# Performance work log

Measured on AMD Instinct MI355X. Metric: run time of the kernel, lower is better.

## Reference

```python
import jax, jax.numpy as jnp
import numpy as np

DIM = 1024
LN_EPS = 1e-5


def setup_inputs() -> dict:
    key = jax.random.key(0)
    ks = jax.random.split(key, 6)
    B, S, D = 8, 2048, DIM
    x = jax.random.normal(ks[0], (B, S, D), dtype=jnp.float32)
    mask = jnp.ones((B, S, 1), dtype=jnp.float32)
    # LayerNorm params
    ln_g = jnp.ones((D,), dtype=jnp.float32)
    ln_b = jnp.zeros((D,), dtype=jnp.float32)
    # FeedForward: Linear(D, D) -> GELU -> Linear(D, D); hidden_dim == dim per source
    lim = 1.0 / np.sqrt(D)
    w1 = jax.random.uniform(ks[1], (D, D), jnp.float32, -lim, lim)
    b1 = jax.random.uniform(ks[2], (D,), jnp.float32, -lim, lim)
    w2 = jax.random.uniform(ks[3], (D, D), jnp.float32, -lim, lim)
    b2 = jax.random.uniform(ks[4], (D,), jnp.float32, -lim, lim)
    return {"x": x, "mask": mask, "ln_g": ln_g, "ln_b": ln_b,
            "w1": w1, "b1": b1, "w2": w2, "b2": b2}


def _layernorm(t, g, b):
    mu = jnp.mean(t, axis=-1, keepdims=True)
    var = jnp.mean(jnp.square(t - mu), axis=-1, keepdims=True)
    return (t - mu) * jax.lax.rsqrt(var + LN_EPS) * g + b


def reference(x, mask, ln_g, ln_b, w1, b1, w2, b2):
    # torch.fft(t, signal_ndim=1): FFT over hidden axis (complex input, imag=0)
    ft = jnp.fft.fft(x.astype(jnp.float32), axis=-1)
    # torch.fft(., signal_ndim=2): 2D FFT over (seq, hidden)
    ft = jnp.fft.fft2(ft, axes=(-2, -1))
    ft = ft.real  # [..., 0] slice of the fake-complex tensor
    t = _layernorm(x + ft, ln_g, ln_b)
    # FeedForward: Linear -> GELU(exact) -> Linear (dropout is identity at eval)
    h = jax.nn.gelu(t @ w1 + b1, approximate=False)
    out = h @ w2 + b2
    return out * mask
```

## Files before the change

kernel.cpp:

```cpp
#include <hip/hip_runtime.h>
#include <math.h>

#define DIMD 1024
#define SEQ  2048
#define BATCH 8
#define ROWS (BATCH * SEQ)

#define MF 1152
#define KF 1088

typedef __attribute__((ext_vector_type(8))) short bf16x8;
typedef __attribute__((ext_vector_type(4))) float f32x4;
typedef __attribute__((ext_vector_type(8))) unsigned short ushort8;

__device__ __forceinline__ unsigned short f2bf(float f) {
    unsigned u = __float_as_uint(f);
    unsigned r = (u + 0x7FFFu + ((u >> 16) & 1u)) >> 16;
    return (unsigned short)r;
}
__device__ __forceinline__ float bf2f(unsigned short h) {
    return __uint_as_float(((unsigned)h) << 16);
}
__device__ __forceinline__ void gl_lds16(const void* g, void* l) {
    __builtin_amdgcn_global_load_lds(
        (const __attribute__((address_space(1))) unsigned int*)g,
        (__attribute__((address_space(3))) unsigned int*)l, 16, 0, 0);
}


__global__ __launch_bounds__(256) void build_acos(unsigned short* __restrict__ Acos) {
    int s = blockIdx.x;
    for (int t = threadIdx.x; t < KF; t += 256) {
        float c = 0.0f;
        if (t <= 1024) {
            int prod = (s * t) & (SEQ - 1);
            c = 1024.0f * cospif((float)prod * (1.0f / 1024.0f));
        }
        Acos[(size_t)s * KF + t] = f2bf(c);
    }
}

__global__ __launch_bounds__(256) void build_xe(const float* __restrict__ x,
                                                unsigned short* __restrict__ Xe) {
    int lane = threadIdx.x & 63;
    int oct  = threadIdx.x >> 6;
    int n = blockIdx.x * 64 + lane;
    int b = n >> 10, d = n & 1023;
    int rd = (DIMD - d) & (DIMD - 1);
    int t0 = blockIdx.y * 32 + oct * 8;
    const float* xb = x + (size_t)b * SEQ * DIMD + rd;
    ushort8 tmp;
    #pragma unroll
    for (int j = 0; j < 8; ++j) {
        int t = t0 + j;
        float v;
        if (t == 0)          v = xb[0];
        else if (t < 1024)   v = xb[(size_t)t * DIMD] + xb[(size_t)(2048 - t) * DIMD];
        else if (t == 1024)  v = xb[(size_t)1024 * DIMD];
        else                 v = 0.0f;
        tmp[j] = f2bf(v);
    }
    *(ushort8*)&Xe[(size_t)n * KF + t0] = tmp;
}

__global__ __launch_bounds__(256) void pack_wt(const float* __restrict__ W,
                                               unsigned short* __restrict__ Wt) {
    int lane = threadIdx.x & 63;
    int oct = threadIdx.x >> 6;
    int n = blockIdx.x * 64 + lane;
    int k0 = blockIdx.y * 32 + oct * 8;
    ushort8 tmp;
    #pragma unroll
    for (int j = 0; j < 8; ++j) tmp[j] = f2bf(W[(size_t)(k0 + j) * DIMD + n]);
    *(ushort8*)&Wt[(size_t)n * DIMD + k0] = tmp;
}

template <int MODE>
__global__ __launch_bounds__(256) void gemm_bt(const unsigned short* __restrict__ A,
                                               const unsigned short* __restrict__ B,
                                               int K, int lda, int ldb, int ldc,
                                               const float* __restrict__ bias,
                                               const float* __restrict__ mask,
                                               void* __restrict__ outp) {
    __shared__ unsigned short As[128 * 64];
    __shared__ unsigned short Bs[128 * 64];

    const int tid = threadIdx.x;
    const int lane = tid & 63;
    const int wv = tid >> 6;
    const int wm = wv & 1;
    const int wn = wv >> 1;
    const int fr = lane & 15;
    const int quad = lane >> 4;

    int bx = blockIdx.x, by = blockIdx.y;
    if (MODE != 0) {
        int lin = bx + 8 * by;
        int c = lin & 7;
        int g = lin >> 3;
        bx = g & 7;
        by = (g >> 3) * 8 + c;
    }
    const int m0 = by * 128;
    const int n0 = bx * 128;

    const int st_row = (lane >> 3);
    const int st_col = ((lane & 7) ^ st_row) * 8;

    f32x4 acc[4][4] = {};

    for (int k0 = 0; k0 < K; k0 += 64) {
        __syncthreads();
        #pragma unroll
        for (int i = 0; i < 4; ++i) {
            int chunk = wv * 4 + i;
            int ar = m0 + chunk * 8 + st_row;
            int br = n0 + chunk * 8 + st_row;
            gl_lds16(&A[(size_t)ar * lda + k0 + st_col], &As[chunk * 512]);
            gl_lds16(&B[(size_t)br * ldb + k0 + st_col], &Bs[chunk * 512]);
        }
        __syncthreads();

        const int sw = fr & 7;
        #pragma unroll
        for (int ks = 0; ks < 2; ++ks) {
            const int slot = (ks * 4 + quad) ^ sw;
            bf16x8 af[4], bfv[4];
            #pragma unroll
            for (int i = 0; i < 4; ++i)
                af[i] = *(const bf16x8*)&As[(wm * 64 + i * 16 + fr) * 64 + slot * 8];
            #pragma unroll
            for (int j = 0; j < 4; ++j)
                bfv[j] = *(const bf16x8*)&Bs[(wn * 64 + j * 16 + fr) * 64 + slot * 8];
            #pragma unroll
            for (int i = 0; i < 4; ++i)
                #pragma unroll
                for (int j = 0; j < 4; ++j)
                    acc[i][j] = __builtin_amdgcn_mfma_f32_16x16x32_bf16(af[i], bfv[j], acc[i][j], 0, 0, 0);
        }
    }

    #pragma unroll
    for (int i = 0; i < 4; ++i) {
        int rowb = m0 + wm * 64 + i * 16 + quad * 4;
        #pragma unroll
        for (int j = 0; j < 4; ++j) {
            int col = n0 + wn * 64 + j * 16 + fr;
            #pragma unroll
            for (int r = 0; r < 4; ++r) {
                float v = acc[i][j][r];
                int row = rowb + r;
                if (MODE == 0) {
                    ((float*)outp)[(size_t)row * ldc + col] = v;
                } else if (MODE == 1) {
                    v += bias[col];
                    v = 0.5f * v * (1.0f + erff(v * 0.70710678118654752f));
                    ((unsigned short*)outp)[(size_t)row * ldc + col] = f2bf(v);
                } else {
                    v += bias[col];
                    v *= mask[row];
                    ((float*)outp)[(size_t)row * ldc + col] = v;
                }
            }
        }
    }
}

__global__ __launch_bounds__(256) void ln_pair(const float* __restrict__ x,
                                               const float* __restrict__ F,
                                               const float* __restrict__ g,
                                               const float* __restrict__ beta,
                                               unsigned short* __restrict__ t) {
    const int sp = blockIdx.x;
    const int b  = blockIdx.y;

    float4 fv = ((const float4*)(F + (size_t)sp * 8192 + (size_t)b * 1024))[threadIdx.x];
    float4 g4 = ((const float4*)g)[threadIdx.x];
    float4 b4 = ((const float4*)beta)[threadIdx.x];

    __shared__ float red[4];
    const int wave = threadIdx.x >> 6;
    const int lane = threadIdx.x & 63;

    const int nrows = (sp >= 1 && sp <= 1023) ? 2 : 1;
    for (int p = 0; p < nrows; ++p) {
        int s = p ? (2048 - sp) : sp;
        int row = b * SEQ + s;
        float4 xv = ((const float4*)(x + (size_t)row * DIMD))[threadIdx.x];
        float v0 = xv.x + fv.x, v1 = xv.y + fv.y, v2 = xv.z + fv.z, v3 = xv.w + fv.w;

        float sm = v0 + v1 + v2 + v3;
        #pragma unroll
        for (int off = 32; off > 0; off >>= 1) sm += __shfl_down(sm, off, 64);
        if (lane == 0) red[wave] = sm;
        __syncthreads();
        const float mean = (red[0] + red[1] + red[2] + red[3]) * (1.0f / DIMD);

        float dx0 = v0 - mean, dx1 = v1 - mean, dx2 = v2 - mean, dx3 = v3 - mean;
        float q = dx0 * dx0 + dx1 * dx1 + dx2 * dx2 + dx3 * dx3;
        __syncthreads();
        #pragma unroll
        for (int off = 32; off > 0; off >>= 1) q += __shfl_down(q, off, 64);
        if (lane == 0) red[wave] = q;
        __syncthreads();
        const float var = (red[0] + red[1] + red[2] + red[3]) * (1.0f / DIMD);
        const float rstd = rsqrtf(var + 1e-5f);

        ushort4 o;
        o.x = f2bf(dx0 * rstd * g4.x + b4.x);
        o.y = f2bf(dx1 * rstd * g4.y + b4.y);
        o.z = f2bf(dx2 * rstd * g4.z + b4.z);
        o.w = f2bf(dx3 * rstd * g4.w + b4.w);
        ((ushort4*)(t + (size_t)row * DIMD))[threadIdx.x] = o;
        __syncthreads();
    }
}

#define BM 64
#define BN 64
#define BK 16

__global__ __launch_bounds__(256) void fft_cos_kernel(const float* __restrict__ x,
                                                      float* __restrict__ y) {
    __shared__ float tab[SEQ];
    __shared__ float As[BM][BK + 1];
    __shared__ float Bs[BK][BN + 1];
    const int tid = threadIdx.x;
    const int b = blockIdx.z;
    const int s0 = blockIdx.y * BM;
    const int n0 = blockIdx.x * BN;
    for (int i = tid; i < SEQ; i += 256) tab[i] = cospif((float)i * (1.0f / 1024.0f));
    const int tx = tid & 15;
    const int ty = tid >> 4;
    float acc[4][4] = {};
    const float* Xb = x + (size_t)b * SEQ * DIMD;
    for (int k0 = 0; k0 < SEQ; k0 += BK) {
        __syncthreads();
        for (int f = tid; f < BM * BK; f += 256) {
            int i = f / BK, k = f % BK;
            int prod = (s0 + i) * (k0 + k);
            As[i][k] = tab[prod & (SEQ - 1)];
        }
        for (int f = tid; f < BK * BN; f += 256) {
            int k = f / BN, j = f % BN;
            int d = n0 + j;
            int rd = (DIMD - d) & (DIMD - 1);
            Bs[k][j] = Xb[(size_t)(k0 + k) * DIMD + rd];
        }
        __syncthreads();
        #pragma unroll
        for (int k = 0; k < BK; ++k) {
            float a[4], bv[4];
            #pragma unroll
            for (int i = 0; i < 4; ++i) a[i] = As[ty * 4 + i][k];
            #pragma unroll
            for (int j = 0; j < 4; ++j) bv[j] = Bs[k][tx * 4 + j];
            #pragma unroll
            for (int i = 0; i < 4; ++i)
                #pragma unroll
                for (int j = 0; j < 4; ++j) acc[i][j] += a[i] * bv[j];
        }
    }
    #pragma unroll
    for (int i = 0; i < 4; ++i) {
        int s = s0 + ty * 4 + i;
        #pragma unroll
        for (int j = 0; j < 4; ++j) {
            int d = n0 + tx * 4 + j;
            y[((size_t)b * SEQ + s) * DIMD + d] = Xb[(size_t)s * DIMD + d] + 1024.0f * acc[i][j];
        }
    }
}

__global__ __launch_bounds__(256) void ln_kernel(float* __restrict__ y,
                                                 const float* __restrict__ g,
                                                 const float* __restrict__ beta) {
    const int row = blockIdx.x;
    float4* p = (float4*)(y + (size_t)row * DIMD);
    float4 v = p[threadIdx.x];
    __shared__ float red[4];
    const int wave = threadIdx.x >> 6;
    const int lane = threadIdx.x & 63;
    float s = v.x + v.y + v.z + v.w;
    #pragma unroll
    for (int off = 32; off > 0; off >>= 1) s += __shfl_down(s, off, 64);
    if (lane == 0) red[wave] = s;
    __syncthreads();
    const float mean = (red[0] + red[1] + red[2] + red[3]) * (1.0f / DIMD);
    float dx0 = v.x - mean, dx1 = v.y - mean, dx2 = v.z - mean, dx3 = v.w - mean;
    float q = dx0 * dx0 + dx1 * dx1 + dx2 * dx2 + dx3 * dx3;
    __syncthreads();
    #pragma unroll
    for (int off = 32; off > 0; off >>= 1) q += __shfl_down(q, off, 64);
    if (lane == 0) red[wave] = q;
    __syncthreads();
    const float var = (red[0] + red[1] + red[2] + red[3]) * (1.0f / DIMD);
    const float rstd = rsqrtf(var + 1e-5f);
    float4 g4 = ((const float4*)g)[threadIdx.x];
    float4 b4 = ((const float4*)beta)[threadIdx.x];
    float4 o;
    o.x = dx0 * rstd * g4.x + b4.x;
    o.y = dx1 * rstd * g4.y + b4.y;
    o.z = dx2 * rstd * g4.z + b4.z;
    o.w = dx3 * rstd * g4.w + b4.w;
    p[threadIdx.x] = o;
}

template <int MODE>
__global__ __launch_bounds__(256) void ff_gemm(const float* __restrict__ A,
                                               const float* __restrict__ W,
                                               const float* __restrict__ bias,
                                               const float* __restrict__ mask,
                                               float* __restrict__ out) {
    __shared__ float As[BM][BK + 1];
    __shared__ float Bs[BK][BN + 1];
    const int tid = threadIdx.x;
    const int tx = tid & 15;
    const int ty = tid >> 4;
    const int m0 = blockIdx.y * BM;
    const int n0 = blockIdx.x * BN;
    float acc[4][4] = {};
    for (int k0 = 0; k0 < DIMD; k0 += BK) {
        __syncthreads();
        for (int f = tid; f < BM * BK; f += 256) {
            int i = f / BK, k = f % BK;
            As[i][k] = A[(size_t)(m0 + i) * DIMD + k0 + k];
        }
        for (int f = tid; f < BK * BN; f += 256) {
            int k = f / BN, j = f % BN;
            Bs[k][j] = W[(size_t)(k0 + k) * DIMD + n0 + j];
        }
        __syncthreads();
        #pragma unroll
        for (int k = 0; k < BK; ++k) {
            float a[4], bv[4];
            #pragma unroll
            for (int i = 0; i < 4; ++i) a[i] = As[ty * 4 + i][k];
            #pragma unroll
            for (int j = 0; j < 4; ++j) bv[j] = Bs[k][tx * 4 + j];
            #pragma unroll
            for (int i = 0; i < 4; ++i)
                #pragma unroll
                for (int j = 0; j < 4; ++j) acc[i][j] += a[i] * bv[j];
        }
    }
    #pragma unroll
    for (int i = 0; i < 4; ++i) {
        int m = m0 + ty * 4 + i;
        float mk = (MODE == 1) ? mask[m] : 1.0f;
        #pragma unroll
        for (int j = 0; j < 4; ++j) {
            int n = n0 + tx * 4 + j;
            float v = acc[i][j] + bias[n];
            if (MODE == 0) v = 0.5f * v * (1.0f + erff(v * 0.70710678118654752f));
            else v *= mk;
            out[(size_t)m * DIMD + n] = v;
        }
    }
}

extern "C" void kernel_launch(void* const* d_in, const int* in_sizes, int n_in,
                              void* d_out, int out_size, void* d_ws, size_t ws_size,
                              hipStream_t stream) {
    const float* x    = (const float*)d_in[0];
    const float* mask = (const float*)d_in[1];
    const float* ln_g = (const float*)d_in[2];
    const float* ln_b = (const float*)d_in[3];
    const float* w1   = (const float*)d_in[4];
    const float* b1   = (const float*)d_in[5];
    const float* w2   = (const float*)d_in[6];
    const float* b2   = (const float*)d_in[7];
    float* out = (float*)d_out;

    const size_t MB = 1024 * 1024;
    dim3 blk(256);

    if (ws_size >= 70 * MB) {
        char* w = (char*)d_ws;
        unsigned short* Acos = (unsigned short*)w;
        unsigned short* Xe   = (unsigned short*)(w + 4 * MB);
        unsigned short* t    = (unsigned short*)(w + 32 * MB);
        unsigned short* h    = (unsigned short*)w;
        unsigned short* W1t  = (unsigned short*)(w + 64 * MB);
        unsigned short* W2t  = (unsigned short*)(w + 66 * MB);
        float* F = (float*)d_out;

        build_acos<<<dim3(MF), blk, 0, stream>>>(Acos);
        build_xe<<<dim3(8192 / 64, KF / 32), blk, 0, stream>>>(x, Xe);
        pack_wt<<<dim3(1024 / 64, 1024 / 32), blk, 0, stream>>>(w1, W1t);
        pack_wt<<<dim3(1024 / 64, 1024 / 32), blk, 0, stream>>>(w2, W2t);

        gemm_bt<0><<<dim3(8192 / 128, MF / 128), blk, 0, stream>>>(
            Acos, Xe, KF, KF, KF, 8192, nullptr, nullptr, F);
        ln_pair<<<dim3(1025, BATCH), blk, 0, stream>>>(x, F, ln_g, ln_b, t);
        gemm_bt<1><<<dim3(1024 / 128, ROWS / 128), blk, 0, stream>>>(
            t, W1t, 1024, 1024, 1024, 1024, b1, nullptr, h);
        gemm_bt<2><<<dim3(1024 / 128, ROWS / 128), blk, 0, stream>>>(
            h, W2t, 1024, 1024, 1024, 1024, b2, mask, out);
    } else {
        float* yf = (float*)d_ws;
        const size_t bufBytes = (size_t)ROWS * DIMD * sizeof(float);
        fft_cos_kernel<<<dim3(DIMD / BN, SEQ / BM, BATCH), blk, 0, stream>>>(x, yf);
        ln_kernel<<<dim3(ROWS), blk, 0, stream>>>(yf, ln_g, ln_b);
        ff_gemm<0><<<dim3(DIMD / BN, ROWS / BM), blk, 0, stream>>>(yf, w1, b1, nullptr, out);
        ff_gemm<1><<<dim3(DIMD / BN, ROWS / BM), blk, 0, stream>>>(out, w2, b2, mask, yf);
        hipMemcpyAsync(d_out, yf, bufBytes, hipMemcpyDeviceToDevice, stream);
    }
}
```

Measured before the change: 333.5 us.

## Replace 128x128 GEMM with 256x256 eight-wave ping-pong pipelined GEMM

Replaces the single-buffered 128x128-tile bf16 MFMA GEMM with a 512-thread, 256x256-tile kernel. It double-buffers LDS, interleaves global-to-LDS staging with MFMA phases, and uses explicit waitcnt, barriers and setprio. The DFT GEMM dimensions are padded to multiples of 256/128 (MF 1280, KF 1152) to fit the new tile, which adds some padded work. The intent is to hide load latency and raise data reuse per tile, at the cost of fewer blocks, higher LDS and register use, and fragile hand-tuned synchronisation.

New measurement: 321.8 us. 3.5% less time.

```diff
diff --git a/kernel.cpp b/kernel.cpp
--- a/kernel.cpp
+++ b/kernel.cpp
@@ -6,8 +6,8 @@
 #define BATCH 8
 #define ROWS (BATCH * SEQ)
 
-#define MF 1152
-#define KF 1088
+#define MF 1280
+#define KF 1152
 
 typedef __attribute__((ext_vector_type(8))) short bf16x8;
 typedef __attribute__((ext_vector_type(4))) float f32x4;
@@ -17,9 +17,6 @@
     unsigned u = __float_as_uint(f);
     unsigned r = (u + 0x7FFFu + ((u >> 16) & 1u)) >> 16;
     return (unsigned short)r;
-}
-__device__ __forceinline__ float bf2f(unsigned short h) {
-    return __uint_as_float(((unsigned)h) << 16);
 }
 __device__ __forceinline__ void gl_lds16(const void* g, void* l) {
     __builtin_amdgcn_global_load_lds(
@@ -76,88 +73,124 @@
 }
 
 template <int MODE>
-__global__ __launch_bounds__(256) void gemm_bt(const unsigned short* __restrict__ A,
-                                               const unsigned short* __restrict__ B,
-                                               int K, int lda, int ldb, int ldc,
-                                               const float* __restrict__ bias,
-                                               const float* __restrict__ mask,
-                                               void* __restrict__ outp) {
-    __shared__ unsigned short As[128 * 64];
-    __shared__ unsigned short Bs[128 * 64];
-
-    const int tid = threadIdx.x;
+__global__ __launch_bounds__(512, 2) void gemm8p(const unsigned short* __restrict__ A,
+                                                 const unsigned short* __restrict__ B,
+                                                 int K, int lda, int ldb, int ldc,
+                                                 const float* __restrict__ bias,
+                                                 const float* __restrict__ mask,
+                                                 void* __restrict__ outp) {
+    __shared__ unsigned short As[2][256 * 64];
+    __shared__ unsigned short Bs[2][256 * 64];
+
+    const int tid  = threadIdx.x;
     const int lane = tid & 63;
-    const int wv = tid >> 6;
-    const int wm = wv & 1;
-    const int wn = wv >> 1;
-    const int fr = lane & 15;
+    const int w    = tid >> 6;
+    const int wm   = w >> 2;
+    const int wn   = w & 3;
+    const int fr   = lane & 15;
     const int quad = lane >> 4;
+    const int sw   = fr & 7;
+
+    const int st_row = lane >> 3;
+    const int st_col = ((lane & 7) ^ st_row) * 8;
 
     int bx = blockIdx.x, by = blockIdx.y;
     if (MODE != 0) {
-        int lin = bx + 8 * by;
-        int c = lin & 7;
-        int g = lin >> 3;
-        bx = g & 7;
-        by = (g >> 3) * 8 + c;
-    }
-    const int m0 = by * 128;
-    const int n0 = bx * 128;
-
-    const int st_row = (lane >> 3);
-    const int st_col = ((lane & 7) ^ st_row) * 8;
-
-    f32x4 acc[4][4] = {};
-
-    for (int k0 = 0; k0 < K; k0 += 64) {
-        __syncthreads();
-        #pragma unroll
-        for (int i = 0; i < 4; ++i) {
-            int chunk = wv * 4 + i;
-            int ar = m0 + chunk * 8 + st_row;
-            int br = n0 + chunk * 8 + st_row;
-            gl_lds16(&A[(size_t)ar * lda + k0 + st_col], &As[chunk * 512]);
-            gl_lds16(&B[(size_t)br * ldb + k0 + st_col], &Bs[chunk * 512]);
-        }
-        __syncthreads();
-
-        const int sw = fr & 7;
-        #pragma unroll
-        for (int ks = 0; ks < 2; ++ks) {
-            const int slot = (ks * 4 + quad) ^ sw;
-            bf16x8 af[4], bfv[4];
-            #pragma unroll
-            for (int i = 0; i < 4; ++i)
-                af[i] = *(const bf16x8*)&As[(wm * 64 + i * 16 + fr) * 64 + slot * 8];
-            #pragma unroll
-            for (int j = 0; j < 4; ++j)
-                bfv[j] = *(const bf16x8*)&Bs[(wn * 64 + j * 16 + fr) * 64 + slot * 8];
-            #pragma unroll
-            for (int i = 0; i < 4; ++i)
-                #pragma unroll
-                for (int j = 0; j < 4; ++j)
-                    acc[i][j] = __builtin_amdgcn_mfma_f32_16x16x32_bf16(af[i], bfv[j], acc[i][j], 0, 0, 0);
-        }
-    }
-
-    #pragma unroll
-    for (int i = 0; i < 4; ++i) {
-        int rowb = m0 + wm * 64 + i * 16 + quad * 4;
-        #pragma unroll
-        for (int j = 0; j < 4; ++j) {
-            int col = n0 + wn * 64 + j * 16 + fr;
+        int lin = bx + 4 * by;
+        int c = lin & 7, r = lin >> 3;
+        by = c * 8 + (r >> 2);
+        bx = r & 3;
+    }
+    const int m0 = by * 256;
+    const int n0 = bx * 256;
+
+    auto stageA = [&](int buf, int qm, int kt) {
+        int kb = kt * 64 + st_col;
+        int c0 = qm * 8 + w;
+        int c1 = 16 + qm * 8 + w;
+        gl_lds16(&A[(size_t)(m0 + c0 * 8 + st_row) * lda + kb], &As[buf][c0 * 512]);
+        gl_lds16(&A[(size_t)(m0 + c1 * 8 + st_row) * lda + kb], &As[buf][c1 * 512]);
+    };
+    auto stageB = [&](int buf, int qn, int kt) {
+        int kb = kt * 64 + st_col;
+        int c0 = (w >> 1) * 8 + qn * 4 + (w & 1) * 2;
+        int c1 = c0 + 1;
+        gl_lds16(&B[(size_t)(n0 + c0 * 8 + st_row) * ldb + kb], &Bs[buf][c0 * 512]);
+        gl_lds16(&B[(size_t)(n0 + c1 * 8 + st_row) * ldb + kb], &Bs[buf][c1 * 512]);
+    };
+
+    f32x4 acc[8][4] = {};
+
+#define PHASE(BUF, QM, QN, STAGE, DOVM)                                              \
+    {                                                                                \
+        bf16x8 af[4][2], bv[2][2];                                                   \
+        _Pragma("unroll") for (int i = 0; i < 4; ++i) {                              \
+            const unsigned short* ab = &As[BUF][(wm * 128 + QM * 64 + i * 16 + fr) * 64]; \
+            _Pragma("unroll") for (int ks = 0; ks < 2; ++ks)                         \
+                af[i][ks] = *(const bf16x8*)&ab[((ks * 4 + quad) ^ sw) * 8];         \
+        }                                                                            \
+        _Pragma("unroll") for (int j = 0; j < 2; ++j) {                              \
+            const unsigned short* bb = &Bs[BUF][(wn * 64 + QN * 32 + j * 16 + fr) * 64]; \
+            _Pragma("unroll") for (int ks = 0; ks < 2; ++ks)                         \
+                bv[j][ks] = *(const bf16x8*)&bb[((ks * 4 + quad) ^ sw) * 8];         \
+        }                                                                            \
+        STAGE;                                                                       \
+        asm volatile("s_waitcnt lgkmcnt(8)");                                        \
+        __builtin_amdgcn_s_barrier();                                                \
+        asm volatile("s_waitcnt lgkmcnt(0)");                                        \
+        __builtin_amdgcn_s_setprio(1);                                               \
+        _Pragma("unroll") for (int i = 0; i < 4; ++i)                                \
+            _Pragma("unroll") for (int j = 0; j < 2; ++j)                            \
+                _Pragma("unroll") for (int ks = 0; ks < 2; ++ks)                     \
+                    acc[QM * 4 + i][QN * 2 + j] = __builtin_amdgcn_mfma_f32_16x16x32_bf16( \
+                        af[i][ks], bv[j][ks], acc[QM * 4 + i][QN * 2 + j], 0, 0, 0); \
+        __builtin_amdgcn_s_setprio(0);                                               \
+        if (DOVM) asm volatile("s_waitcnt vmcnt(4)" ::: "memory");                   \
+        __builtin_amdgcn_s_barrier();                                                \
+    }
+
+    const int NT  = K >> 6;
+    const int NIT = NT >> 1;
+
+    stageA(0, 0, 0); stageB(0, 0, 0); stageA(0, 1, 0); stageB(0, 1, 0);
+    stageA(1, 0, 1); stageB(1, 0, 1);
+    asm volatile("s_waitcnt vmcnt(4)" ::: "memory");
+    __builtin_amdgcn_s_barrier();
+
+    for (int i = 0; i < NIT; ++i) {
+        int t1 = 2 * i + 1;
+        int t2 = 2 * i + 2; if (t2 >= NT) t2 = NT - 2;
+        int t3 = 2 * i + 3; if (t3 >= NT) t3 = NT - 2;
+        PHASE(0, 0, 0, stageA(1, 1, t1), 0)
+        PHASE(0, 0, 1, stageB(1, 1, t1), 0)
+        PHASE(0, 1, 0, stageA(0, 0, t2), 0)
+        PHASE(0, 1, 1, stageB(0, 0, t2), 1)
+        PHASE(1, 0, 0, stageA(0, 1, t2), 0)
+        PHASE(1, 0, 1, stageB(0, 1, t2), 0)
+        PHASE(1, 1, 0, stageA(1, 0, t3), 0)
+        PHASE(1, 1, 1, stageB(1, 0, t3), 1)
+    }
+#undef PHASE
+
+    #pragma unroll
+    for (int mi = 0; mi < 8; ++mi) {
+        int rowb = m0 + wm * 128 + mi * 16 + quad * 4;
+        #pragma unroll
+        for (int nj = 0; nj < 4; ++nj) {
+            int col = n0 + wn * 64 + nj * 16 + fr;
+            float bcol = (MODE != 0) ? bias[col] : 0.0f;
             #pragma unroll
             for (int r = 0; r < 4; ++r) {
-                float v = acc[i][j][r];
+                float v = acc[mi][nj][r];
                 int row = rowb + r;
                 if (MODE == 0) {
                     ((float*)outp)[(size_t)row * ldc + col] = v;
                 } else if (MODE == 1) {
-                    v += bias[col];
+                    v += bcol;
                     v = 0.5f * v * (1.0f + erff(v * 0.70710678118654752f));
                     ((unsigned short*)outp)[(size_t)row * ldc + col] = f2bf(v);
                 } else {
-                    v += bias[col];
+                    v += bcol;
                     v *= mask[row];
                     ((float*)outp)[(size_t)row * ldc + col] = v;
                 }
@@ -374,6 +407,7 @@
 
     const size_t MB = 1024 * 1024;
     dim3 blk(256);
+    dim3 blk512(512);
 
     if (ws_size >= 70 * MB) {
         char* w = (char*)d_ws;
@@ -390,12 +424,12 @@
         pack_wt<<<dim3(1024 / 64, 1024 / 32), blk, 0, stream>>>(w1, W1t);
         pack_wt<<<dim3(1024 / 64, 1024 / 32), blk, 0, stream>>>(w2, W2t);
 
-        gemm_bt<0><<<dim3(8192 / 128, MF / 128), blk, 0, stream>>>(
+        gemm8p<0><<<dim3(8192 / 256, MF / 256), blk512, 0, stream>>>(
             Acos, Xe, KF, KF, KF, 8192, nullptr, nullptr, F);
         ln_pair<<<dim3(1025, BATCH), blk, 0, stream>>>(x, F, ln_g, ln_b, t);
-        gemm_bt<1><<<dim3(1024 / 128, ROWS / 128), blk, 0, stream>>>(
+        gemm8p<1><<<dim3(1024 / 256, ROWS / 256), blk512, 0, stream>>>(
             t, W1t, 1024, 1024, 1024, 1024, b1, nullptr, h);
-        gemm_bt<2><<<dim3(1024 / 128, ROWS / 128), blk, 0, stream>>>(
+        gemm8p<2><<<dim3(1024 / 256, ROWS / 256), blk512, 0, stream>>>(
             h, W2t, 1024, 1024, 1024, 1024, b2, mask, out);
     } else {
         float* yf = (float*)d_ws;
```
